# Kernel tuning notes

Hardware: AMD Instinct MI355X
Metric: run time of the kernel (lower is better)

The kernel has to match this reference:

```python
import jax, jax.numpy as jnp
import numpy as np


def setup_inputs() -> dict:
    key = jax.random.key(0)
    k1, k2 = jax.random.split(key)
    # x: (B, C, D, H, W); w: (out_ch, C * 2*2*2)
    x = jax.random.normal(k1, (4, 64, 33, 33, 33), dtype=jnp.float32)
    w = jax.random.normal(k2, (128, 64 * 8), dtype=jnp.float32) * 0.05
    return {"x": x, "w": w}


def reference(x, w):
    # unfoldNd(kernel=2, stride=1, pad=0) + einsum('ij,kjm->kim', w, patches)
    # is exactly a valid 3D cross-correlation with a 2x2x2 kernel.
    B, C, D, H, W = x.shape
    O = w.shape[0]
    kern = w.reshape(O, C, 2, 2, 2)  # unfold flattening order: (C, kd, kh, kw)
    y = jax.lax.conv_general_dilated(
        x, kern,
        window_strides=(1, 1, 1),
        padding='VALID',
        dimension_numbers=('NCDHW', 'OIDHW', 'NCDHW'),
    )  # (B, O, D-1, H-1, W-1)
    return (y + 1.0) ** 2
```

## Files before the change

### kernel.cpp

```cpp
#include <hip/hip_runtime.h>

typedef __bf16 bf16x8 __attribute__((ext_vector_type(8)));
typedef float f32x4 __attribute__((ext_vector_type(4)));
typedef unsigned short u16;
typedef unsigned int u32;
typedef u32 u32x4 __attribute__((ext_vector_type(4)));
typedef u16 u16x8 __attribute__((ext_vector_type(8)));

#define AS1 __attribute__((address_space(1)))
#define AS3 __attribute__((address_space(3)))
#define GLL16(gp, lp) __builtin_amdgcn_global_load_lds((const AS1 void*)(gp), (AS3 void*)(lp), 16, 0, 0)

__device__ __forceinline__ u16 f32_to_bf16_rne(float f) {
    union { float f; unsigned u; } cv; cv.f = f;
    unsigned u = cv.u;
    return (u16)((u + 0x7FFFu + ((u >> 16) & 1u)) >> 16);
}

__device__ __forceinline__ u32 cvt_pk_bf16(float lo, float hi) {
    u32 r;
    asm("v_cvt_pk_bf16_f32 %0, %1, %2" : "=v"(r) : "v"(lo), "v"(hi));
    return r;
}

__global__ void repack_w_kernel(const float* __restrict__ w, u16* __restrict__ w3) {
    int e = blockIdx.x * 256 + threadIdx.x;
    int j    = e & 7;
    int g    = (e >> 3) & 3;
    int o    = (e >> 5) & 127;
    int cb   = (e >> 12) & 1;
    int koff = (e >> 13) & 7;
    int c = (cb << 5) + (g << 3) + j;
    w3[e] = f32_to_bf16_rne(w[(o << 9) + (c << 3) + koff]);
}

__global__ __launch_bounds__(256) void transpose_x_kernel(
    const float* __restrict__ x, u16* __restrict__ xT, u16* __restrict__ x32) {

    const int bid = blockIdx.x;
    const int h = bid % 33;
    const int dq = bid / 33;
    const int d = dq % 33;
    const int b = dq / 33;
    const float* xp = x + (size_t)b * 2299968 + d * 1089 + h * 33;

    const int tid = threadIdx.x;
    const int wv  = tid & 31;
    const int cc  = tid >> 5;
    const float* p = xp + (size_t)cc * 8 * 35937 + wv;
    float f0 = p[0],              f1 = p[35937],          f2 = p[2 * 35937], f3 = p[3 * 35937];
    float f4 = p[(size_t)4*35937],f5 = p[(size_t)5*35937],f6 = p[(size_t)6*35937],f7 = p[(size_t)7*35937];
    u32x4 v;
    v[0] = cvt_pk_bf16(f0, f1);
    v[1] = cvt_pk_bf16(f2, f3);
    v[2] = cvt_pk_bf16(f4, f5);
    v[3] = cvt_pk_bf16(f6, f7);
    *reinterpret_cast<u32x4*>(&xT[(size_t)bid * 2048 + cc * 256 + wv * 8]) = v;

    if (tid < 8) {
        const float* q = xp + (size_t)tid * 8 * 35937 + 32;
        u32x4 m;
        m[0] = cvt_pk_bf16(q[0],              q[35937]);
        m[1] = cvt_pk_bf16(q[2 * 35937],      q[3 * 35937]);
        m[2] = cvt_pk_bf16(q[(size_t)4*35937],q[(size_t)5*35937]);
        m[3] = cvt_pk_bf16(q[(size_t)6*35937],q[(size_t)7*35937]);
        *reinterpret_cast<u32x4*>(&x32[(size_t)bid * 64 + tid * 8]) = m;
    }
}

__global__ __launch_bounds__(512, 4) void conv_mfma_kernel(
    const u16* __restrict__ xT, const u16* __restrict__ x32,
    const u16* __restrict__ w3, float* __restrict__ out) {

    __shared__ __align__(16) u16 xs[19008];

    const int tid = threadIdx.x;
    const int bid = blockIdx.x;
    const int hy0 = (bid & 15) << 1;
    const int dz0 = ((bid >> 4) & 15) << 1;
    const int b   = bid >> 8;

    const int lane = tid & 63;
    const int ln   = lane & 15;
    const int g    = lane >> 4;
    const int o0   = (tid >> 6) << 4;

    bf16x8 wreg[8][2];
#pragma unroll
    for (int koff = 0; koff < 8; ++koff)
#pragma unroll
        for (int cb = 0; cb < 2; ++cb) {
            const u16* p = w3 + ((size_t)((((koff << 1) + cb) * 128) + o0 + ln) << 5) + (g << 3);
            wreg[koff][cb] = __builtin_bit_cast(bf16x8, *reinterpret_cast<const u16x8*>(p));
        }

    char* ldsb = (char*)xs;
    const int slab0 = b * 1089 + dz0 * 33 + hy0;
#pragma unroll
    for (int r = 0; r < 5; ++r) {
        if (r == 4 && tid >= 256) continue;
        const int u   = tid + (r << 9);
        const int sid = u >> 8;
        const int s   = (sid * 171) >> 9;
        const int hh  = sid - s * 3;
        const char* src = (const char*)xT + ((size_t)(slab0 + s * 33 + hh) << 12)
                          + ((u & 255) << 4);
        GLL16(src, ldsb + (u << 4));
    }
    if (tid < 72) {
        const int s  = (tid * 171) >> 12;
        const int rr = tid - s * 24;
        const char* src = (const char*)x32
            + ((size_t)(b * 1089 + (dz0 + s) * 33 + hy0) << 7) + (rr << 4);
        GLL16(src, ldsb + 36864 + (tid << 4));
    }
    asm volatile("s_waitcnt vmcnt(0)" ::: "memory");
    __syncthreads();

    f32x4 acc[2][4];
#pragma unroll
    for (int od = 0; od < 2; ++od)
#pragma unroll
        for (int mf = 0; mf < 4; ++mf)
            acc[od][mf] = (f32x4){0.f, 0.f, 0.f, 0.f};

#pragma unroll
    for (int s = 0; s < 3; ++s) {
#pragma unroll
        for (int cb = 0; cb < 2; ++cb) {
            const int cc = (cb << 2) + g;
#pragma unroll
            for (int kw = 0; kw < 2; ++kw) {
#pragma unroll
                for (int hh = 0; hh < 3; ++hh) {
                    bf16x8 xf[2];
#pragma unroll
                    for (int wh = 0; wh < 2; ++wh) {
                        const int row = (wh << 4) + ln + kw;
                        const u16* p = (row < 32)
                            ? &xs[((s * 3 + hh) << 11) + (cc << 8) + (row << 3)]
                            : &xs[18432 + s * 192 + hh * 64 + (cc << 3)];
                        xf[wh] = __builtin_bit_cast(bf16x8,
                            *reinterpret_cast<const u16x8*>(p));
                    }
#pragma unroll
                    for (int kh = 0; kh < 2; ++kh) {
                        const int hrow = hh - kh;
                        if (hrow < 0 || hrow > 1) continue;
                        const int kk = (kh << 1) + kw;
#pragma unroll
                        for (int wh = 0; wh < 2; ++wh) {
                            const int mf = (hrow << 1) + wh;
                            if (s < 2)
                                acc[s][mf] = __builtin_amdgcn_mfma_f32_16x16x32_bf16(
                                    wreg[kk][cb], xf[wh], acc[s][mf], 0, 0, 0);
                            if (s >= 1)
                                acc[s - 1][mf] = __builtin_amdgcn_mfma_f32_16x16x32_bf16(
                                    wreg[4 + kk][cb], xf[wh], acc[s - 1][mf], 0, 0, 0);
                        }
                    }
                }
            }
        }
    }

    float* ob = out + (size_t)b * 128 * 32768 + ((size_t)dz0 << 10) + (hy0 << 5);
#pragma unroll
    for (int mf = 0; mf < 4; ++mf) {
        const int wx   = ((mf & 1) << 4) + ln;
        const int hrow = mf >> 1;
#pragma unroll
        for (int r = 0; r < 4; ++r) {
            const int n = o0 + (g << 2) + r;
            float* o2 = ob + ((size_t)n << 15) + (hrow << 5) + wx;
            float v0 = acc[0][mf][r] + 1.0f;
            o2[0] = v0 * v0;
            float v1 = acc[1][mf][r] + 1.0f;
            o2[1024] = v1 * v1;
        }
    }
}

#define XS_ROW 72
__global__ __launch_bounds__(256, 4) void conv_mfma_fallback(
    const float* __restrict__ x, const u16* __restrict__ w3, float* __restrict__ out) {

    __shared__ __align__(16) u16 xs[6 * 33 * XS_ROW];

    const int tid = threadIdx.x;
    const int bid = blockIdx.x;
    const int hy0 = (bid & 15) << 1;
    const int dz  = (bid >> 4) & 31;
    const int b   = bid >> 9;

    const float* xb = x + (size_t)b * 64 * 35937;
    for (int i = tid; i < 1584; i += 256) {
        int w   = i % 33;
        int t   = i / 33;
        int q   = t & 7;
        int kh3 = t >> 3;
        int kd  = kh3 >= 3 ? 1 : 0;
        int kh  = kh3 - kd * 3;
        const float* p = xb + (size_t)(q << 3) * 35937 + (dz + kd) * 1089 + (hy0 + kh) * 33 + w;
        u32x4 v;
        v[0] = cvt_pk_bf16(p[0], p[35937]);
        v[1] = cvt_pk_bf16(p[2 * 35937], p[3 * 35937]);
        v[2] = cvt_pk_bf16(p[4 * 35937], p[5 * 35937]);
        v[3] = cvt_pk_bf16(p[6 * 35937], p[7 * 35937]);
        *reinterpret_cast<u32x4*>(&xs[(kh3 * 33 + w) * XS_ROW + (q << 3)]) = v;
    }
    __syncthreads();

    const int lane = tid & 63;
    const int ln   = lane & 15;
    const int g    = lane >> 4;
    const int n0w  = (tid >> 6) << 5;

    f32x4 acc[2][4];
#pragma unroll
    for (int nf = 0; nf < 2; ++nf)
#pragma unroll
        for (int mf = 0; mf < 4; ++mf)
            acc[nf][mf] = (f32x4){0.f, 0.f, 0.f, 0.f};

#pragma unroll
    for (int cb = 0; cb < 2; ++cb) {
        const int cbase = (cb << 5) + (g << 3);
#pragma unroll
        for (int kd = 0; kd < 2; ++kd) {
            bf16x8 wf[2][4];
#pragma unroll
            for (int nf = 0; nf < 2; ++nf)
#pragma unroll
                for (int kk = 0; kk < 4; ++kk) {
                    const int koff = (kd << 2) + kk;
                    const u16* p = w3 + (size_t)((((koff << 1) + cb) << 7)
                                   + n0w + (nf << 4) + ln) * 32 + (g << 3);
                    wf[nf][kk] = __builtin_bit_cast(bf16x8, *reinterpret_cast<const u16x8*>(p));
                }
#pragma unroll
            for (int kw = 0; kw < 2; ++kw) {
                bf16x8 xf[3][2];
#pragma unroll
                for (int hh = 0; hh < 3; ++hh)
#pragma unroll
                    for (int wh = 0; wh < 2; ++wh) {
                        const int row = (kd * 3 + hh) * 33 + (wh << 4) + ln + kw;
                        xf[hh][wh] = __builtin_bit_cast(bf16x8,
                            *reinterpret_cast<const u16x8*>(&xs[row * XS_ROW + cbase]));
                    }
#pragma unroll
                for (int kh = 0; kh < 2; ++kh)
#pragma unroll
                    for (int nf = 0; nf < 2; ++nf)
#pragma unroll
                        for (int mf = 0; mf < 4; ++mf)
                            acc[nf][mf] = __builtin_amdgcn_mfma_f32_16x16x32_bf16(
                                wf[nf][(kh << 1) + kw], xf[(mf >> 1) + kh][mf & 1],
                                acc[nf][mf], 0, 0, 0);
            }
        }
    }

    float* ob = out + ((size_t)b * 128) * 32768 + (dz << 10) + (hy0 << 5);
#pragma unroll
    for (int nf = 0; nf < 2; ++nf)
#pragma unroll
        for (int mf = 0; mf < 4; ++mf) {
            const int wx   = ((mf & 1) << 4) + ln;
            const int hrow = mf >> 1;
            float* o2 = ob + (hrow << 5) + wx;
#pragma unroll
            for (int r = 0; r < 4; ++r) {
                const int n = n0w + (nf << 4) + (g << 2) + r;
                float v = acc[nf][mf][r] + 1.0f;
                o2[(size_t)n << 15] = v * v;
            }
        }
}

extern "C" void kernel_launch(void* const* d_in, const int* in_sizes, int n_in,
                              void* d_out, int out_size, void* d_ws, size_t ws_size,
                              hipStream_t stream) {
    const float* x = (const float*)d_in[0];
    const float* w = (const float*)d_in[1];
    float* out = (float*)d_out;

    const size_t W3_BYTES  = 131072;
    const size_t XT_BYTES  = (size_t)4356 * 4096;
    const size_t X32_BYTES = (size_t)4356 * 128;
    const size_t NEED = W3_BYTES + XT_BYTES + X32_BYTES;

    u16* w3 = (u16*)d_ws;
    repack_w_kernel<<<256, 256, 0, stream>>>(w, w3);

    if (ws_size >= NEED) {
        u16* xT  = (u16*)((char*)d_ws + W3_BYTES);
        u16* x32 = (u16*)((char*)d_ws + W3_BYTES + XT_BYTES);
        transpose_x_kernel<<<4356, 256, 0, stream>>>(x, xT, x32);
        conv_mfma_kernel<<<1024, 512, 0, stream>>>(xT, x32, w3, out);
    } else {
        conv_mfma_fallback<<<2048, 256, 0, stream>>>(x, w3, out);
    }
}
```

Measured before the change: 52.04 us.

## Switch conv kernel to 32x32x16 MFMA with per-warp hrow split and streamed weights

Replaces the 16x16x32 MFMA tiling with 32x32x16 bf16 MFMAs. Each wave now covers 32 output channels by one h-row by 32 w positions, and a new repack kernel lays weights out to match. Weights are no longer preloaded into registers; they are loaded from global/L2 inside the loop, which lowers register pressure and the number of MFMA issues. The cost is repeated weight fetches per block and a different LDS read pattern.

```diff
diff --git a/kernel.cpp b/kernel.cpp
--- a/kernel.cpp
+++ b/kernel.cpp
@@ -2,6 +2,7 @@
 
 typedef __bf16 bf16x8 __attribute__((ext_vector_type(8)));
 typedef float f32x4 __attribute__((ext_vector_type(4)));
+typedef float f32x16 __attribute__((ext_vector_type(16)));
 typedef unsigned short u16;
 typedef unsigned int u32;
 typedef u32 u32x4 __attribute__((ext_vector_type(4)));
@@ -21,6 +22,17 @@
     u32 r;
     asm("v_cvt_pk_bf16_f32 %0, %1, %2" : "=v"(r) : "v"(lo), "v"(hi));
     return r;
+}
+
+__global__ void repack_w4_kernel(const float* __restrict__ w, u16* __restrict__ w4) {
+    int e = blockIdx.x * 256 + threadIdx.x;
+    int j    = e & 7;
+    int half = (e >> 3) & 1;
+    int o    = (e >> 4) & 127;
+    int cq   = (e >> 11) & 3;
+    int koff = (e >> 13) & 7;
+    int c = cq * 16 + half * 8 + j;
+    w4[e] = f32_to_bf16_rne(w[(o << 9) + (c << 3) + koff]);
 }
 
 __global__ void repack_w_kernel(const float* __restrict__ w, u16* __restrict__ w3) {
@@ -70,7 +82,7 @@
 
 __global__ __launch_bounds__(512, 4) void conv_mfma_kernel(
     const u16* __restrict__ xT, const u16* __restrict__ x32,
-    const u16* __restrict__ w3, float* __restrict__ out) {
+    const u16* __restrict__ w4, float* __restrict__ out) {
 
     __shared__ __align__(16) u16 xs[19008];
 
@@ -79,20 +91,6 @@
     const int hy0 = (bid & 15) << 1;
     const int dz0 = ((bid >> 4) & 15) << 1;
     const int b   = bid >> 8;
-
-    const int lane = tid & 63;
-    const int ln   = lane & 15;
-    const int g    = lane >> 4;
-    const int o0   = (tid >> 6) << 4;
-
-    bf16x8 wreg[8][2];
-#pragma unroll
-    for (int koff = 0; koff < 8; ++koff)
-#pragma unroll
-        for (int cb = 0; cb < 2; ++cb) {
-            const u16* p = w3 + ((size_t)((((koff << 1) + cb) * 128) + o0 + ln) << 5) + (g << 3);
-            wreg[koff][cb] = __builtin_bit_cast(bf16x8, *reinterpret_cast<const u16x8*>(p));
-        }
 
     char* ldsb = (char*)xs;
     const int slab0 = b * 1089 + dz0 * 33 + hy0;
@@ -117,68 +115,70 @@
     asm volatile("s_waitcnt vmcnt(0)" ::: "memory");
     __syncthreads();
 
-    f32x4 acc[2][4];
+    const int lane = tid & 63;
+    const int l31  = lane & 31;
+    const int half = lane >> 5;
+    const int wid  = tid >> 6;
+    const int o0   = (wid >> 1) << 5;
+    const int hrow = wid & 1;
+
+    f32x16 acc[2];
 #pragma unroll
     for (int od = 0; od < 2; ++od)
 #pragma unroll
-        for (int mf = 0; mf < 4; ++mf)
-            acc[od][mf] = (f32x4){0.f, 0.f, 0.f, 0.f};
-
-#pragma unroll
-    for (int s = 0; s < 3; ++s) {
-#pragma unroll
-        for (int cb = 0; cb < 2; ++cb) {
-            const int cc = (cb << 2) + g;
-#pragma unroll
-            for (int kw = 0; kw < 2; ++kw) {
-#pragma unroll
-                for (int hh = 0; hh < 3; ++hh) {
-                    bf16x8 xf[2];
-#pragma unroll
-                    for (int wh = 0; wh < 2; ++wh) {
-                        const int row = (wh << 4) + ln + kw;
-                        const u16* p = (row < 32)
-                            ? &xs[((s * 3 + hh) << 11) + (cc << 8) + (row << 3)]
-                            : &xs[18432 + s * 192 + hh * 64 + (cc << 3)];
-                        xf[wh] = __builtin_bit_cast(bf16x8,
-                            *reinterpret_cast<const u16x8*>(p));
-                    }
-#pragma unroll
-                    for (int kh = 0; kh < 2; ++kh) {
-                        const int hrow = hh - kh;
-                        if (hrow < 0 || hrow > 1) continue;
-                        const int kk = (kh << 1) + kw;
-#pragma unroll
-                        for (int wh = 0; wh < 2; ++wh) {
-                            const int mf = (hrow << 1) + wh;
-                            if (s < 2)
-                                acc[s][mf] = __builtin_amdgcn_mfma_f32_16x16x32_bf16(
-                                    wreg[kk][cb], xf[wh], acc[s][mf], 0, 0, 0);
-                            if (s >= 1)
-                                acc[s - 1][mf] = __builtin_amdgcn_mfma_f32_16x16x32_bf16(
-                                    wreg[4 + kk][cb], xf[wh], acc[s - 1][mf], 0, 0, 0);
-                        }
-                    }
+        for (int r = 0; r < 16; ++r)
+            acc[od][r] = 0.f;
+
+#pragma unroll
+    for (int kw = 0; kw < 2; ++kw) {
+        const int row = l31 + kw;
+#pragma unroll
+        for (int cq = 0; cq < 4; ++cq) {
+            const int cc = (cq << 1) + half;
+            bf16x8 A[2][2];
+#pragma unroll
+            for (int kd = 0; kd < 2; ++kd)
+#pragma unroll
+                for (int kh = 0; kh < 2; ++kh) {
+                    const int t = (((kd << 2) + (kh << 1) + kw) << 2) + cq;
+                    const u16* p = w4 + (t << 11) + ((o0 + l31) << 4) + (half << 3);
+                    A[kd][kh] = __builtin_bit_cast(bf16x8, *reinterpret_cast<const u16x8*>(p));
                 }
-            }
+            bf16x8 B[3][2];
+#pragma unroll
+            for (int s = 0; s < 3; ++s)
+#pragma unroll
+                for (int kh = 0; kh < 2; ++kh) {
+                    const int hh = hrow + kh;
+                    const u16* p = (row < 32)
+                        ? &xs[((s * 3 + hh) << 11) + (cc << 8) + (row << 3)]
+                        : &xs[18432 + s * 192 + hh * 64 + (cc << 3)];
+                    B[s][kh] = __builtin_bit_cast(bf16x8, *reinterpret_cast<const u16x8*>(p));
+                }
+#pragma unroll
+            for (int s = 0; s < 3; ++s)
+#pragma unroll
+                for (int kh = 0; kh < 2; ++kh) {
+                    if (s < 2)
+                        acc[s] = __builtin_amdgcn_mfma_f32_32x32x16_bf16(
+                            A[0][kh], B[s][kh], acc[s], 0, 0, 0);
+                    if (s >= 1)
+                        acc[s - 1] = __builtin_amdgcn_mfma_f32_32x32x16_bf16(
+                            A[1][kh], B[s][kh], acc[s - 1], 0, 0, 0);
+                }
         }
     }
 
-    float* ob = out + (size_t)b * 128 * 32768 + ((size_t)dz0 << 10) + (hy0 << 5);
-#pragma unroll
-    for (int mf = 0; mf < 4; ++mf) {
-        const int wx   = ((mf & 1) << 4) + ln;
-        const int hrow = mf >> 1;
-#pragma unroll
-        for (int r = 0; r < 4; ++r) {
-            const int n = o0 + (g << 2) + r;
-            float* o2 = ob + ((size_t)n << 15) + (hrow << 5) + wx;
-            float v0 = acc[0][mf][r] + 1.0f;
-            o2[0] = v0 * v0;
-            float v1 = acc[1][mf][r] + 1.0f;
-            o2[1024] = v1 * v1;
+    float* ob = out + (size_t)b * 128 * 32768 + ((size_t)dz0 << 10)
+                + ((hy0 + hrow) << 5) + l31;
+#pragma unroll
+    for (int od = 0; od < 2; ++od)
+#pragma unroll
+        for (int r = 0; r < 16; ++r) {
+            const int orow = (r & 3) + ((r >> 2) << 3) + (half << 2);
+            float v = acc[od][r] + 1.0f;
+            ob[((size_t)(o0 + orow) << 15) + (od << 10)] = v * v;
         }
-    }
 }
 
 #define XS_ROW 72
@@ -245,9 +245,9 @@
                 for (int hh = 0; hh < 3; ++hh)
 #pragma unroll
                     for (int wh = 0; wh < 2; ++wh) {
-                        const int row = (kd * 3 + hh) * 33 + (wh << 4) + ln + kw;
+                        const int rw = (kd * 3 + hh) * 33 + (wh << 4) + ln + kw;
                         xf[hh][wh] = __builtin_bit_cast(bf16x8,
-                            *reinterpret_cast<const u16x8*>(&xs[row * XS_ROW + cbase]));
+                            *reinterpret_cast<const u16x8*>(&xs[rw * XS_ROW + cbase]));
                     }
 #pragma unroll
                 for (int kh = 0; kh < 2; ++kh)
@@ -286,20 +286,21 @@
     const float* w = (const float*)d_in[1];
     float* out = (float*)d_out;
 
-    const size_t W3_BYTES  = 131072;
+    const size_t W_BYTES   = 131072;
     const size_t XT_BYTES  = (size_t)4356 * 4096;
     const size_t X32_BYTES = (size_t)4356 * 128;
-    const size_t NEED = W3_BYTES + XT_BYTES + X32_BYTES;
-
-    u16* w3 = (u16*)d_ws;
-    repack_w_kernel<<<256, 256, 0, stream>>>(w, w3);
+    const size_t NEED = W_BYTES + XT_BYTES + X32_BYTES;
 
     if (ws_size >= NEED) {
-        u16* xT  = (u16*)((char*)d_ws + W3_BYTES);
-        u16* x32 = (u16*)((char*)d_ws + W3_BYTES + XT_BYTES);
+        u16* w4  = (u16*)d_ws;
+        u16* xT  = (u16*)((char*)d_ws + W_BYTES);
+        u16* x32 = (u16*)((char*)d_ws + W_BYTES + XT_BYTES);
+        repack_w4_kernel<<<256, 256, 0, stream>>>(w, w4);
         transpose_x_kernel<<<4356, 256, 0, stream>>>(x, xT, x32);
-        conv_mfma_kernel<<<1024, 512, 0, stream>>>(xT, x32, w3, out);
+        conv_mfma_kernel<<<1024, 512, 0, stream>>>(xT, x32, w4, out);
     } else {
+        u16* w3 = (u16*)d_ws;
+        repack_w_kernel<<<256, 256, 0, stream>>>(w, w3);
         conv_mfma_fallback<<<2048, 256, 0, stream>>>(x, w3, out);
     }
 }
```

New measurement: 49.55 us. 1.05x faster.
